# Kernel optimization log

Hardware: AMD Instinct MI355X
Metric: run time of the kernel (lower is better)

The kernel has to match this reference:

```python
import jax, jax.numpy as jnp
import numpy as np

N_DIM = 256
MAX_LEN = 256


def sincos_embedding(max_len, d):
    # standard transformer sin/cos positional embedding: (max_len, d)
    pos = np.arange(max_len, dtype=np.float32)[:, None]
    i = np.arange(d // 2, dtype=np.float32)
    angle = pos / np.power(10000.0, (2.0 * i) / d)
    pe = np.zeros((max_len, d), dtype=np.float32)
    pe[:, 0::2] = np.sin(angle)
    pe[:, 1::2] = np.cos(angle)
    return jnp.asarray(pe)


def setup_inputs() -> dict:
    key = jax.random.key(0)
    ks = jax.random.split(key, 7)
    B, C, H, W = 64, N_DIM, 8, 32
    s = 1.0 / np.sqrt(N_DIM)
    return {
        "x": jax.random.normal(ks[0], (B, C, H, W), dtype=jnp.float32),
        "seq_len": 26,
        "wo_w": jax.random.normal(ks[1], (N_DIM, N_DIM), dtype=jnp.float32) * s,
        "wo_b": jax.random.normal(ks[2], (N_DIM,), dtype=jnp.float32) * s,
        "wv_w": jax.random.normal(ks[3], (N_DIM, N_DIM), dtype=jnp.float32) * s,
        "wv_b": jax.random.normal(ks[4], (N_DIM,), dtype=jnp.float32) * s,
        "we_w": jax.random.normal(ks[5], (1, N_DIM), dtype=jnp.float32) * s,
        "we_b": jax.random.normal(ks[6], (1,), dtype=jnp.float32) * s,
    }


def reference(x, seq_len, wo_w, wo_b, wv_w, wv_b, we_w, we_b):
    B, C, H, W = x.shape
    D = C
    xh = jnp.transpose(x, (0, 2, 3, 1))  # (B, H, W, D)
    pe = sincos_embedding(MAX_LEN, D)[:seq_len]  # (T, D)
    # reading-state projection: (T, D) -> broadcast over batch
    att_r = pe @ wo_w.T + wo_b  # (T, D)
    # visual-feature projection
    att_x = xh @ wv_w.T + wv_b  # (B, H, W, D)
    # broadcast additive attention: (B, T, H, W, D)
    att = jnp.tanh(att_x[:, None] + att_r[None, :, None, None, :])
    score = jnp.einsum('bthwd,d->bthw', att, we_w[0]) + we_b[0]
    score = score.reshape(B, seq_len, H * W)
    alpha = jax.nn.softmax(score, axis=2)  # (B, T, HW)
    v = att_x.reshape(B, H * W, D)  # values are the wv projection
    # torch does mean over HW of alpha*v -> sum(alpha*v)/HW
    out = jnp.einsum('bts,bsd->btd', alpha, v) / (H * W)
    return out
```

## Files before the change

kernel.cpp:

```cpp
#include <hip/hip_runtime.h>

#define DD 256
#define BB 64
#define SS 256
#define K2 2.8853900817779268f
#define LOG2E 1.4426950408889634f

#if __has_builtin(__builtin_amdgcn_exp2f)
#define EXP2(x) __builtin_amdgcn_exp2f(x)
#else
#define EXP2(x) exp2f(x)
#endif

typedef __attribute__((ext_vector_type(8))) short bf16x8;
typedef __attribute__((ext_vector_type(4))) float f32x4;

static __device__ __forceinline__ float fast_rcp(float x) {
  return __builtin_amdgcn_rcpf(x);
}

__global__ __launch_bounds__(256) void k_prep(
    const float* __restrict__ wo_w, const float* __restrict__ wo_b,
    float* __restrict__ att_r, int T)
{
  const int tid = threadIdx.x;
  const int t = blockIdx.x;
  if (t >= T) return;
  __shared__ float pe[DD];
  {
    int i = tid >> 1;
    double r = pow(10000.0, -(double)(2*i) / 256.0);
    double ang = (double)t * r;
    pe[tid] = (float)((tid & 1) ? cos(ang) : sin(ang));
  }
  __syncthreads();
  const float4* wr = reinterpret_cast<const float4*>(wo_w + (size_t)tid * DD);
  const float4* pp = reinterpret_cast<const float4*>(pe);
  float acc = 0.f;
#pragma unroll 8
  for (int k = 0; k < 64; ++k) {
    float4 w4 = wr[k]; float4 p4 = pp[k];
    acc = fmaf(w4.x, p4.x, acc);
    acc = fmaf(w4.y, p4.y, acc);
    acc = fmaf(w4.z, p4.z, acc);
    acc = fmaf(w4.w, p4.w, acc);
  }
  att_r[(size_t)t*DD + tid] = acc + wo_b[tid];
}

__global__ __launch_bounds__(256) void k_attx(
    const float* __restrict__ x, const float* __restrict__ wv_w,
    const float* __restrict__ wv_b, float* __restrict__ att_x)
{
  const int b   = blockIdx.z;
  const int dT  = blockIdx.y;
  const int s0  = blockIdx.x * 64;
  const int d0  = dT * 128;
  const int tid = threadIdx.x;
  const int lane = tid & 63;
  const int wid  = tid >> 6;
  const float* xb = x + (size_t)b * DD * SS;

  __shared__ float xls[32 * 65];
  __shared__ unsigned short wbh[128 * 32];
  __shared__ unsigned short wbl[128 * 32];

  f32x4 acc[8];
#pragma unroll
  for (int dt = 0; dt < 8; ++dt) acc[dt] = (f32x4){0.f, 0.f, 0.f, 0.f};

  const int dl = tid >> 1, kh = tid & 1;
  const float* wsrc = wv_w + (size_t)(d0 + dl) * DD + kh * 16;
  const int cl = tid >> 3, sq = (tid & 7) * 8;
  const float* xsrc = xb + (size_t)cl * SS + s0 + sq;

  float4 wr0, wr1, wr2, wr3, xr0, xr1;
  wr0 = *reinterpret_cast<const float4*>(wsrc);
  wr1 = *reinterpret_cast<const float4*>(wsrc + 4);
  wr2 = *reinterpret_cast<const float4*>(wsrc + 8);
  wr3 = *reinterpret_cast<const float4*>(wsrc + 12);
  xr0 = *reinterpret_cast<const float4*>(xsrc);
  xr1 = *reinterpret_cast<const float4*>(xsrc + 4);

  for (int cc = 0; cc < 8; ++cc) {
    __syncthreads();
    {
      const float wf[16] = {wr0.x, wr0.y, wr0.z, wr0.w, wr1.x, wr1.y, wr1.z, wr1.w,
                            wr2.x, wr2.y, wr2.z, wr2.w, wr3.x, wr3.y, wr3.z, wr3.w};
      const int dt = dl >> 4, dcol = dl & 15;
#pragma unroll
      for (int g2 = 0; g2 < 2; ++g2) {
        const int kg = kh * 2 + g2;
        unsigned hp[4], lp[4];
#pragma unroll
        for (int p = 0; p < 4; ++p) {
          float fa = wf[g2 * 8 + p * 2], fb = wf[g2 * 8 + p * 2 + 1];
          unsigned ua = __float_as_uint(fa), ub = __float_as_uint(fb);
          hp[p] = (ua >> 16) | (ub & 0xffff0000u);
          float la = fa - __uint_as_float(ua & 0xffff0000u);
          float lb = fb - __uint_as_float(ub & 0xffff0000u);
          lp[p] = (__float_as_uint(la) >> 16) | (__float_as_uint(lb) & 0xffff0000u);
        }
        const int base = ((dt * 4 + kg) * 16 + dcol) * 8;
        *reinterpret_cast<uint4*>(&wbh[base]) = make_uint4(hp[0], hp[1], hp[2], hp[3]);
        *reinterpret_cast<uint4*>(&wbl[base]) = make_uint4(lp[0], lp[1], lp[2], lp[3]);
      }
    }
    {
      float* xd = &xls[cl * 65 + sq];
      xd[0] = xr0.x; xd[1] = xr0.y; xd[2] = xr0.z; xd[3] = xr0.w;
      xd[4] = xr1.x; xd[5] = xr1.y; xd[6] = xr1.z; xd[7] = xr1.w;
    }
    if (cc < 7) {
      const float* wn = wsrc + (size_t)(cc + 1) * 32;
      wr0 = *reinterpret_cast<const float4*>(wn);
      wr1 = *reinterpret_cast<const float4*>(wn + 4);
      wr2 = *reinterpret_cast<const float4*>(wn + 8);
      wr3 = *reinterpret_cast<const float4*>(wn + 12);
      const float* xn = xsrc + (size_t)(cc + 1) * 32 * SS;
      xr0 = *reinterpret_cast<const float4*>(xn);
      xr1 = *reinterpret_cast<const float4*>(xn + 4);
    }
    __syncthreads();
    const int g = lane >> 4;
    const int sA = wid * 16 + (lane & 15);
    union { bf16x8 v; unsigned short u[8]; } ah, al;
#pragma unroll
    for (int j = 0; j < 8; ++j) {
      float f = xls[(g * 8 + j) * 65 + sA];
      unsigned u = __float_as_uint(f);
      ah.u[j] = (unsigned short)(u >> 16);
      float fl = f - __uint_as_float(u & 0xffff0000u);
      al.u[j] = (unsigned short)(__float_as_uint(fl) >> 16);
    }
#pragma unroll
    for (int dt = 0; dt < 8; ++dt) {
      const int base = ((dt * 4 + g) * 16 + (lane & 15)) * 8;
      bf16x8 bh = *reinterpret_cast<const bf16x8*>(&wbh[base]);
      bf16x8 bl = *reinterpret_cast<const bf16x8*>(&wbl[base]);
      acc[dt] = __builtin_amdgcn_mfma_f32_16x16x32_bf16(ah.v, bh, acc[dt], 0, 0, 0);
      acc[dt] = __builtin_amdgcn_mfma_f32_16x16x32_bf16(ah.v, bl, acc[dt], 0, 0, 0);
      acc[dt] = __builtin_amdgcn_mfma_f32_16x16x32_bf16(al.v, bh, acc[dt], 0, 0, 0);
    }
  }

  const int dcol = lane & 15, rg = lane >> 4;
#pragma unroll
  for (int dt = 0; dt < 8; ++dt) {
    const int d = d0 + dt * 16 + dcol;
    float bv = wv_b[d];
#pragma unroll
    for (int r = 0; r < 4; ++r) {
      const int s = s0 + wid * 16 + rg * 4 + r;
      att_x[((size_t)(b * SS + s)) * DD + d] = acc[dt][r] + bv;
    }
  }
}

__global__ __launch_bounds__(1024, 2) void k_score_out(
    const float* __restrict__ att_x, const float* __restrict__ att_r,
    const float* __restrict__ we_w, float* __restrict__ out, int T)
{
  const int b  = blockIdx.x;
  const int tq = blockIdx.y;
  const int tchunk = (T + 3) >> 2;
  const int t0 = tq * tchunk;
  const int nT = (T - t0 < tchunk) ? (T - t0) : tchunk;
  if (nT <= 0) return;
  const int tid = threadIdx.x;

  __shared__ float pool[4096];
  __shared__ float scS[8 * 256];
  __shared__ float mred[8][4];
  __shared__ float sred[8][4];

  for (int idx = tid; idx < nT * 256; idx += 1024) {
    int tl = idx >> 8, d = idx & 255;
    pool[tl * 320 + (d >> 4) * 20 + (d & 15)] = EXP2(att_r[(size_t)(t0 + tl) * DD + d] * K2);
  }
  for (int idx = tid; idx < 8 * 256; idx += 1024) scS[idx] = 0.f;

  const int sl = tid >> 4;
  const int c  = tid & 15;
  float4 w0, w1, w2, w3;
  {
    const float4* we4 = reinterpret_cast<const float4*>(we_w + c * 16);
    w0 = we4[0]; w1 = we4[1]; w2 = we4[2]; w3 = we4[3];
  }
  __syncthreads();

#pragma unroll
  for (int q = 0; q < 4; ++q) {
    const int s = q * 64 + sl;
    float f0x, f0y, f0z, f0w, f1x, f1y, f1z, f1w;
    float f2x, f2y, f2z, f2w, f3x, f3y, f3z, f3w;
    {
      const float4* ax4 = reinterpret_cast<const float4*>(
          att_x + ((size_t)(b * SS + s)) * DD + c * 16);
      float4 a = ax4[0], bq = ax4[1], cq = ax4[2], dq = ax4[3];
      f0x = EXP2(a.x*K2);  f0y = EXP2(a.y*K2);  f0z = EXP2(a.z*K2);  f0w = EXP2(a.w*K2);
      f1x = EXP2(bq.x*K2); f1y = EXP2(bq.y*K2); f1z = EXP2(bq.z*K2); f1w = EXP2(bq.w*K2);
      f2x = EXP2(cq.x*K2); f2y = EXP2(cq.y*K2); f2z = EXP2(cq.z*K2); f2w = EXP2(cq.w*K2);
      f3x = EXP2(dq.x*K2); f3y = EXP2(dq.y*K2); f3z = EXP2(dq.z*K2); f3w = EXP2(dq.w*K2);
    }
#pragma unroll 2
    for (int tl = 0; tl < nT; ++tl) {
      const float* aS = &pool[tl * 320 + c * 20];
      float4 a0 = *reinterpret_cast<const float4*>(aS);
      float4 a1 = *reinterpret_cast<const float4*>(aS + 4);
      float4 a2 = *reinterpret_cast<const float4*>(aS + 8);
      float4 a3 = *reinterpret_cast<const float4*>(aS + 12);
      float p0 = 0.f, p1 = 0.f, p2 = 0.f, p3 = 0.f;
      p0 = fmaf(w0.x, fast_rcp(fmaf(f0x, a0.x, 1.f)), p0);
      p0 = fmaf(w0.y, fast_rcp(fmaf(f0y, a0.y, 1.f)), p0);
      p0 = fmaf(w0.z, fast_rcp(fmaf(f0z, a0.z, 1.f)), p0);
      p0 = fmaf(w0.w, fast_rcp(fmaf(f0w, a0.w, 1.f)), p0);
      p1 = fmaf(w1.x, fast_rcp(fmaf(f1x, a1.x, 1.f)), p1);
      p1 = fmaf(w1.y, fast_rcp(fmaf(f1y, a1.y, 1.f)), p1);
      p1 = fmaf(w1.z, fast_rcp(fmaf(f1z, a1.z, 1.f)), p1);
      p1 = fmaf(w1.w, fast_rcp(fmaf(f1w, a1.w, 1.f)), p1);
      p2 = fmaf(w2.x, fast_rcp(fmaf(f2x, a2.x, 1.f)), p2);
      p2 = fmaf(w2.y, fast_rcp(fmaf(f2y, a2.y, 1.f)), p2);
      p2 = fmaf(w2.z, fast_rcp(fmaf(f2z, a2.z, 1.f)), p2);
      p2 = fmaf(w2.w, fast_rcp(fmaf(f2w, a2.w, 1.f)), p2);
      p3 = fmaf(w3.x, fast_rcp(fmaf(f3x, a3.x, 1.f)), p3);
      p3 = fmaf(w3.y, fast_rcp(fmaf(f3y, a3.y, 1.f)), p3);
      p3 = fmaf(w3.z, fast_rcp(fmaf(f3z, a3.z, 1.f)), p3);
      p3 = fmaf(w3.w, fast_rcp(fmaf(f3w, a3.w, 1.f)), p3);
      float part = (p0 + p1) + (p2 + p3);
      part += __shfl_xor(part, 1);
      part += __shfl_xor(part, 2);
      part += __shfl_xor(part, 4);
      part += __shfl_xor(part, 8);
      if (c == 0) scS[tl * 256 + s] = -2.f * part;
    }
  }
  __syncthreads();

  const int d   = tid & 255;
  const int scg = tid >> 8;
  const int wv4 = d >> 6;
#pragma unroll
  for (int pass = 0; pass < 2; ++pass) {
    const int r = pass * 4 + scg;
    const bool live = (r < nT);
    float v = live ? scS[r * 256 + d] : -3.0e38f;
    float m = v;
    m = fmaxf(m, __shfl_xor(m, 1));
    m = fmaxf(m, __shfl_xor(m, 2));
    m = fmaxf(m, __shfl_xor(m, 4));
    m = fmaxf(m, __shfl_xor(m, 8));
    m = fmaxf(m, __shfl_xor(m, 16));
    m = fmaxf(m, __shfl_xor(m, 32));
    if ((tid & 63) == 0) mred[r][wv4] = m;
    __syncthreads();
    float M = fmaxf(fmaxf(mred[r][0], mred[r][1]), fmaxf(mred[r][2], mred[r][3]));
    float ev = live ? EXP2((v - M) * LOG2E) : 0.f;
    float ss = ev;
    ss += __shfl_xor(ss, 1);
    ss += __shfl_xor(ss, 2);
    ss += __shfl_xor(ss, 4);
    ss += __shfl_xor(ss, 8);
    ss += __shfl_xor(ss, 16);
    ss += __shfl_xor(ss, 32);
    if ((tid & 63) == 0) sred[r][wv4] = ss;
    __syncthreads();
    float S = sred[r][0] + sred[r][1] + sred[r][2] + sred[r][3];
    if (live) scS[r * 256 + d] = ev * fast_rcp(S);
  }
  __syncthreads();

  float v[64];
  const float* ax = att_x + ((size_t)(b * SS) + scg * 64) * DD + d;
#pragma unroll
  for (int i = 0; i < 64; ++i) v[i] = ax[(size_t)i * DD];

#pragma unroll
  for (int half = 0; half < 2; ++half) {
    const int nR = (nT - half * 4 < 4) ? (nT - half * 4) : 4;
#pragma unroll
    for (int tl = 0; tl < 4; ++tl) {
      float a = 0.f;
#pragma unroll
      for (int i4 = 0; i4 < 16; ++i4) {
        float4 a4 = *reinterpret_cast<const float4*>(
            &scS[(half * 4 + tl) * 256 + scg * 64 + i4 * 4]);
        a = fmaf(a4.x, v[i4*4+0], a);
        a = fmaf(a4.y, v[i4*4+1], a);
        a = fmaf(a4.z, v[i4*4+2], a);
        a = fmaf(a4.w, v[i4*4+3], a);
      }
      pool[scg * 1024 + tl * 256 + d] = a;
    }
    __syncthreads();
    for (int idx = tid; idx < nR * 256; idx += 1024) {
      float sum = pool[idx] + pool[1024 + idx] + pool[2048 + idx] + pool[3072 + idx];
      out[((size_t)b * T + t0 + half * 4) * SS + idx] = sum * (1.0f / 256.0f);
    }
    __syncthreads();
  }
}

extern "C" void kernel_launch(void* const* d_in, const int* in_sizes, int n_in,
                              void* d_out, int out_size, void* d_ws, size_t ws_size,
                              hipStream_t stream) {
  (void)in_sizes; (void)n_in; (void)ws_size;
  const float* x    = (const float*)d_in[0];
  const float* wo_w = (const float*)d_in[2];
  const float* wo_b = (const float*)d_in[3];
  const float* wv_w = (const float*)d_in[4];
  const float* wv_b = (const float*)d_in[5];
  const float* we_w = (const float*)d_in[6];
  float* out = (float*)d_out;
  const int T = out_size / (BB * DD);

  float* att_x = (float*)d_ws;
  float* att_r = att_x + (size_t)BB * SS * DD;

  k_prep      <<<dim3(T), 256, 0, stream>>>(wo_w, wo_b, att_r, T);
  k_attx      <<<dim3(4, 2, BB), 256, 0, stream>>>(x, wv_w, wv_b, att_x);
  k_score_out <<<dim3(BB, 4), 1024, 0, stream>>>(att_x, att_r, we_w, out, T);
}
```

Before: 56.17 us.

## Pre-split wv_w into bf16 hi/lo fragments once and drop LDS staging in attx

The prep kernel gains 8 extra blocks that convert wv_w into MFMA-ready bf16 hi/lo fragment layouts in workspace, once per call. The projection kernel then reads those fragments and x columns straight from global memory, with no shared-memory staging or barriers. It also splits D into four 64-wide tiles, doubling the grid. This trades repeated per-block weight conversion and LDS traffic for uncoalesced, strided global loads of x and redundant fragment reads that rely on the cache.

Result: slower. 57.76 us (+2.8%).

```diff
diff --git a/kernel.cpp b/kernel.cpp
--- a/kernel.cpp
+++ b/kernel.cpp
@@ -20,11 +20,42 @@
 }
 
 __global__ __launch_bounds__(256) void k_prep(
+    const float* __restrict__ wv_w,
     const float* __restrict__ wo_w, const float* __restrict__ wo_b,
+    unsigned short* __restrict__ whi, unsigned short* __restrict__ wlo,
     float* __restrict__ att_r, int T)
 {
   const int tid = threadIdx.x;
-  const int t = blockIdx.x;
+  if (blockIdx.x < 8) {
+    const int cc = blockIdx.x;
+#pragma unroll
+    for (int sl = 0; sl < 4; ++sl) {
+      const int slot = sl * 256 + tid;
+      const int dt16 = slot >> 6;
+      const int kg   = (slot >> 4) & 3;
+      const int dcol = slot & 15;
+      const int d  = dt16 * 16 + dcol;
+      const int c0 = cc * 32 + kg * 8;
+      float4 a = *reinterpret_cast<const float4*>(wv_w + (size_t)d * DD + c0);
+      float4 b4 = *reinterpret_cast<const float4*>(wv_w + (size_t)d * DD + c0 + 4);
+      const float wf[8] = {a.x, a.y, a.z, a.w, b4.x, b4.y, b4.z, b4.w};
+      unsigned hp[4], lp[4];
+#pragma unroll
+      for (int p = 0; p < 4; ++p) {
+        float fa = wf[p * 2], fb = wf[p * 2 + 1];
+        unsigned ua = __float_as_uint(fa), ub = __float_as_uint(fb);
+        hp[p] = (ua >> 16) | (ub & 0xffff0000u);
+        float la = fa - __uint_as_float(ua & 0xffff0000u);
+        float lb = fb - __uint_as_float(ub & 0xffff0000u);
+        lp[p] = (__float_as_uint(la) >> 16) | (__float_as_uint(lb) & 0xffff0000u);
+      }
+      const size_t base = ((size_t)cc * 1024 + slot) * 8;
+      *reinterpret_cast<uint4*>(whi + base) = make_uint4(hp[0], hp[1], hp[2], hp[3]);
+      *reinterpret_cast<uint4*>(wlo + base) = make_uint4(lp[0], lp[1], lp[2], lp[3]);
+    }
+    return;
+  }
+  const int t = blockIdx.x - 8;
   if (t >= T) return;
   __shared__ float pe[DD];
   {
@@ -49,110 +80,55 @@
 }
 
 __global__ __launch_bounds__(256) void k_attx(
-    const float* __restrict__ x, const float* __restrict__ wv_w,
+    const float* __restrict__ x,
+    const unsigned short* __restrict__ whi, const unsigned short* __restrict__ wlo,
     const float* __restrict__ wv_b, float* __restrict__ att_x)
 {
   const int b   = blockIdx.z;
-  const int dT  = blockIdx.y;
+  const int dq  = blockIdx.y;
   const int s0  = blockIdx.x * 64;
-  const int d0  = dT * 128;
   const int tid = threadIdx.x;
   const int lane = tid & 63;
   const int wid  = tid >> 6;
-  const float* xb = x + (size_t)b * DD * SS;
-
-  __shared__ float xls[32 * 65];
-  __shared__ unsigned short wbh[128 * 32];
-  __shared__ unsigned short wbl[128 * 32];
-
-  f32x4 acc[8];
-#pragma unroll
-  for (int dt = 0; dt < 8; ++dt) acc[dt] = (f32x4){0.f, 0.f, 0.f, 0.f};
-
-  const int dl = tid >> 1, kh = tid & 1;
-  const float* wsrc = wv_w + (size_t)(d0 + dl) * DD + kh * 16;
-  const int cl = tid >> 3, sq = (tid & 7) * 8;
-  const float* xsrc = xb + (size_t)cl * SS + s0 + sq;
-
-  float4 wr0, wr1, wr2, wr3, xr0, xr1;
-  wr0 = *reinterpret_cast<const float4*>(wsrc);
-  wr1 = *reinterpret_cast<const float4*>(wsrc + 4);
-  wr2 = *reinterpret_cast<const float4*>(wsrc + 8);
-  wr3 = *reinterpret_cast<const float4*>(wsrc + 12);
-  xr0 = *reinterpret_cast<const float4*>(xsrc);
-  xr1 = *reinterpret_cast<const float4*>(xsrc + 4);
-
+  const int g    = lane >> 4;
+  const int scol = lane & 15;
+  const float* xcol = x + (size_t)b * DD * SS + s0 + wid * 16 + scol;
+
+  f32x4 acc[4];
+#pragma unroll
+  for (int dtl = 0; dtl < 4; ++dtl) acc[dtl] = (f32x4){0.f, 0.f, 0.f, 0.f};
+
+#pragma unroll
   for (int cc = 0; cc < 8; ++cc) {
-    __syncthreads();
-    {
-      const float wf[16] = {wr0.x, wr0.y, wr0.z, wr0.w, wr1.x, wr1.y, wr1.z, wr1.w,
-                            wr2.x, wr2.y, wr2.z, wr2.w, wr3.x, wr3.y, wr3.z, wr3.w};
-      const int dt = dl >> 4, dcol = dl & 15;
-#pragma unroll
-      for (int g2 = 0; g2 < 2; ++g2) {
-        const int kg = kh * 2 + g2;
-        unsigned hp[4], lp[4];
-#pragma unroll
-        for (int p = 0; p < 4; ++p) {
-          float fa = wf[g2 * 8 + p * 2], fb = wf[g2 * 8 + p * 2 + 1];
-          unsigned ua = __float_as_uint(fa), ub = __float_as_uint(fb);
-          hp[p] = (ua >> 16) | (ub & 0xffff0000u);
-          float la = fa - __uint_as_float(ua & 0xffff0000u);
-          float lb = fb - __uint_as_float(ub & 0xffff0000u);
-          lp[p] = (__float_as_uint(la) >> 16) | (__float_as_uint(lb) & 0xffff0000u);
-        }
-        const int base = ((dt * 4 + kg) * 16 + dcol) * 8;
-        *reinterpret_cast<uint4*>(&wbh[base]) = make_uint4(hp[0], hp[1], hp[2], hp[3]);
-        *reinterpret_cast<uint4*>(&wbl[base]) = make_uint4(lp[0], lp[1], lp[2], lp[3]);
-      }
-    }
-    {
-      float* xd = &xls[cl * 65 + sq];
-      xd[0] = xr0.x; xd[1] = xr0.y; xd[2] = xr0.z; xd[3] = xr0.w;
-      xd[4] = xr1.x; xd[5] = xr1.y; xd[6] = xr1.z; xd[7] = xr1.w;
-    }
-    if (cc < 7) {
-      const float* wn = wsrc + (size_t)(cc + 1) * 32;
-      wr0 = *reinterpret_cast<const float4*>(wn);
-      wr1 = *reinterpret_cast<const float4*>(wn + 4);
-      wr2 = *reinterpret_cast<const float4*>(wn + 8);
-      wr3 = *reinterpret_cast<const float4*>(wn + 12);
-      const float* xn = xsrc + (size_t)(cc + 1) * 32 * SS;
-      xr0 = *reinterpret_cast<const float4*>(xn);
-      xr1 = *reinterpret_cast<const float4*>(xn + 4);
-    }
-    __syncthreads();
-    const int g = lane >> 4;
-    const int sA = wid * 16 + (lane & 15);
     union { bf16x8 v; unsigned short u[8]; } ah, al;
 #pragma unroll
     for (int j = 0; j < 8; ++j) {
-      float f = xls[(g * 8 + j) * 65 + sA];
+      float f = xcol[(size_t)(cc * 32 + g * 8 + j) * SS];
       unsigned u = __float_as_uint(f);
       ah.u[j] = (unsigned short)(u >> 16);
       float fl = f - __uint_as_float(u & 0xffff0000u);
       al.u[j] = (unsigned short)(__float_as_uint(fl) >> 16);
     }
 #pragma unroll
-    for (int dt = 0; dt < 8; ++dt) {
-      const int base = ((dt * 4 + g) * 16 + (lane & 15)) * 8;
-      bf16x8 bh = *reinterpret_cast<const bf16x8*>(&wbh[base]);
-      bf16x8 bl = *reinterpret_cast<const bf16x8*>(&wbl[base]);
-      acc[dt] = __builtin_amdgcn_mfma_f32_16x16x32_bf16(ah.v, bh, acc[dt], 0, 0, 0);
-      acc[dt] = __builtin_amdgcn_mfma_f32_16x16x32_bf16(ah.v, bl, acc[dt], 0, 0, 0);
-      acc[dt] = __builtin_amdgcn_mfma_f32_16x16x32_bf16(al.v, bh, acc[dt], 0, 0, 0);
+    for (int dtl = 0; dtl < 4; ++dtl) {
+      const size_t base = ((size_t)cc * 1024 + (size_t)(dq * 4 + dtl) * 64 + lane) * 8;
+      bf16x8 bh = *reinterpret_cast<const bf16x8*>(whi + base);
+      bf16x8 bl = *reinterpret_cast<const bf16x8*>(wlo + base);
+      acc[dtl] = __builtin_amdgcn_mfma_f32_16x16x32_bf16(ah.v, bh, acc[dtl], 0, 0, 0);
+      acc[dtl] = __builtin_amdgcn_mfma_f32_16x16x32_bf16(ah.v, bl, acc[dtl], 0, 0, 0);
+      acc[dtl] = __builtin_amdgcn_mfma_f32_16x16x32_bf16(al.v, bh, acc[dtl], 0, 0, 0);
     }
   }
 
   const int dcol = lane & 15, rg = lane >> 4;
 #pragma unroll
-  for (int dt = 0; dt < 8; ++dt) {
-    const int d = d0 + dt * 16 + dcol;
+  for (int dtl = 0; dtl < 4; ++dtl) {
+    const int d = dq * 64 + dtl * 16 + dcol;
     float bv = wv_b[d];
 #pragma unroll
     for (int r = 0; r < 4; ++r) {
       const int s = s0 + wid * 16 + rg * 4 + r;
-      att_x[((size_t)(b * SS + s)) * DD + d] = acc[dt][r] + bv;
+      att_x[((size_t)(b * SS + s)) * DD + d] = acc[dtl][r] + bv;
     }
   }
 }
@@ -316,8 +292,10 @@
 
   float* att_x = (float*)d_ws;
   float* att_r = att_x + (size_t)BB * SS * DD;
-
-  k_prep      <<<dim3(T), 256, 0, stream>>>(wo_w, wo_b, att_r, T);
-  k_attx      <<<dim3(4, 2, BB), 256, 0, stream>>>(x, wv_w, wv_b, att_x);
+  unsigned short* whi = (unsigned short*)(att_r + 32 * DD);
+  unsigned short* wlo = whi + 65536;
+
+  k_prep      <<<dim3(8 + T), 256, 0, stream>>>(wv_w, wo_w, wo_b, whi, wlo, att_r, T);
+  k_attx      <<<dim3(4, 4, BB), 256, 0, stream>>>(x, whi, wlo, wv_b, att_x);
   k_score_out <<<dim3(BB, 4), 1024, 0, stream>>>(att_x, att_r, we_w, out, T);
 }
```
